# Kernel tuning notes

Hardware: AMD Instinct MI355X
Metric: run time of the kernel (lower is better)

The kernel has to match this reference:

```python
import jax, jax.numpy as jnp
import numpy as np

N, DEG, FIN, FOUT, K = 50000, 16, 32, 64, 3
E = N * DEG


def setup_inputs() -> dict:
    key = jax.random.key(0)
    ks = jax.random.split(key, 10)
    rng = np.random.default_rng(0)
    # unique edges sorted row-major (src*N+dst), ring guarantees deg_in/out>0
    ring = np.arange(N, dtype=np.int64) * N + (np.arange(N, dtype=np.int64) + 1) % N
    cand = np.unique(rng.integers(0, N * N, size=3 * E, dtype=np.int64))
    cand = np.setdiff1d(cand, ring, assume_unique=True)[: E - N]
    codes = np.sort(np.concatenate([cand, ring]))
    assert codes.shape[0] == E
    edge_index = jnp.asarray(np.stack([codes // N, codes % N]).astype(np.int32))
    X = jax.random.normal(ks[0], (N, FIN), jnp.float32)
    edge_weight = jax.random.uniform(ks[1], (E,), jnp.float32, 0.5, 1.5)
    cin = FIN + FOUT
    xav = float(np.sqrt(6.0 / (cin + FOUT)))
    def w(k):
        return jax.random.uniform(k, (2, K, cin, FOUT), jnp.float32, -xav, xav)
    return {
        'X': X, 'edge_index': edge_index, 'edge_weight': edge_weight,
        'Wz': w(ks[2]), 'bz': jnp.zeros((FOUT,), jnp.float32),
        'Wr': w(ks[3]), 'br': jnp.zeros((FOUT,), jnp.float32),
        'Wh': w(ks[4]), 'bh': jnp.zeros((FOUT,), jnp.float32),
    }


def _dconv(X, src, dst, rev_src, rev_dst, norm_out, norm_in, W, b):
    n = X.shape[0]
    def prop(x, s, d, nrm):  # out[d] += nrm * x[s]
        return jax.ops.segment_sum(nrm[:, None] * x[s], d, num_segments=n)
    H = X @ W[0, 0] + X @ W[1, 0]
    if W.shape[1] > 1:
        Tx1o = prop(X, src, dst, norm_out)
        Tx1i = prop(X, rev_src, rev_dst, norm_in)
        H = H + Tx1o @ W[0, 1] + Tx1i @ W[1, 1]
        for k in range(2, W.shape[1]):
            Tx1o = 2.0 * prop(Tx1o, src, dst, norm_out) - X
            Tx1i = 2.0 * prop(Tx1i, rev_src, rev_dst, norm_in) - X
            H = H + Tx1o @ W[0, k] + Tx1i @ W[1, k]
    return H + b


def reference(X, edge_index, edge_weight, Wz, bz, Wr, br, Wh, bh):
    n = X.shape[0]
    src, dst = edge_index[0], edge_index[1]
    deg_out = jax.ops.segment_sum(edge_weight, src, num_segments=n)
    deg_in = jax.ops.segment_sum(edge_weight, dst, num_segments=n)
    # faithful to original: both norms indexed by row (source)
    norm_out = 1.0 / deg_out[src]
    norm_in = 1.0 / deg_in[src]
    # reverse edges in dense_to_sparse(adj.T) order: sorted by (dst, src)
    order = jnp.argsort(dst.astype(jnp.int64) * n + src.astype(jnp.int64))
    rev_src, rev_dst = dst[order], src[order]
    H = jnp.zeros((n, Wz.shape[-1]), X.dtype)
    dc = lambda inp, W, b: _dconv(inp, src, dst, rev_src, rev_dst, norm_out, norm_in, W, b)
    Z = jax.nn.sigmoid(dc(jnp.concatenate([X, H], axis=1), Wz, bz))
    R = jax.nn.sigmoid(dc(jnp.concatenate([X, H], axis=1), Wr, br))
    H_tilde = jnp.tanh(dc(jnp.concatenate([X, H * R], axis=1), Wh, bh))
    return Z * H + (1.0 - Z) * H_tilde
```

## Files before the change

kernel.cpp:

```cpp
#include <hip/hip_runtime.h>
#include <hip/hip_fp16.h>
#include <cmath>

#define NN 50000
#define NE 800000
#define NBIN 391
#define NBLK 391
#define FCAP 3072
#define DST_HI 42949
#define SRC_CUT 33648

__device__ __forceinline__ unsigned short f2h(float f) {
  __half h = __float2half_rn(f);
  return *reinterpret_cast<unsigned short*>(&h);
}

typedef _Float16 half4 __attribute__((ext_vector_type(4)));
typedef float f32x4 __attribute__((ext_vector_type(4)));

__global__ __launch_bounds__(256) void k_aux(const float* __restrict__ X, const int* __restrict__ src,
                                             const int* __restrict__ dst, const float* __restrict__ ew,
                                             int* __restrict__ H,
                                             int* __restrict__ rptr, float* __restrict__ dout,
                                             const float* __restrict__ Wz, const float* __restrict__ Wh,
                                             unsigned short* __restrict__ WT, unsigned short* __restrict__ Xh,
                                             int* __restrict__ s0g) {
  __shared__ int hh[NBIN];
  __shared__ int s0l;
  int bid = blockIdx.x;
  int t = threadIdx.x;
  if (bid >= 667) {
    int h = bid - 667;
    hh[t] = 0;
    if (t + 256 < NBIN) hh[t + 256] = 0;
    if (t == 0) s0l = 0;
    __syncthreads();
    int my = 0;
#pragma unroll
    for (int r = 0; r < 8; ++r) {
      int e = h * 2048 + r * 256 + t;
      if (e < NE) {
        int d = dst[e];
        atomicAdd(&hh[d >> 7], 1);
        my += (d < DST_HI) ? 1 : 0;
        my += (d == DST_HI && src[e] < SRC_CUT) ? 1 : 0;
      }
    }
    atomicAdd(&s0l, my);
    __syncthreads();
    H[t * NBLK + h] = hh[t];
    if (t + 256 < NBIN) H[(t + 256) * NBLK + h] = hh[t + 256];
    if (t == 0) atomicAdd(s0g, s0l);
  } else if (bid < 196) {
    int i = bid * 256 + t;
    if (i >= NN) return;
    int lo = 0, hi = NE;
    while (lo < hi) { int m = (lo + hi) >> 1; if (src[m] < i) lo = m + 1; else hi = m; }
    int lo2 = lo, hi2 = NE;
    while (lo2 < hi2) { int m = (lo2 + hi2) >> 1; if (src[m] < i + 1) lo2 = m + 1; else hi2 = m; }
    rptr[i] = lo;
    if (i == NN - 1) rptr[NN] = lo2;
    float a = 0.f;
    for (int p = lo; p < lo2; ++p) a += ew[p];
    dout[i] = a;
  } else if (bid < 276) {
    int idx = (bid - 196) * 256 + t;
    int kk = idx >> 7, f = idx & 127;
    int blk = kk >> 5, c = kk & 31;
    const float* W = (f < 64) ? Wz : Wh;
    int fl = f & 63;
    float v;
    if (blk == 0)      v = W[c * 64 + fl] + W[18432 + c * 64 + fl];
    else if (blk == 1) v = W[6144 + c * 64 + fl];
    else if (blk == 2) v = W[18432 + 6144 + c * 64 + fl];
    else if (blk == 3) v = W[2 * 6144 + c * 64 + fl];
    else               v = W[18432 + 2 * 6144 + c * 64 + fl];
    WT[f * 160 + kk] = f2h(v);
  } else {
    int tt = (bid - 276) * 256 + t;
    int base = tt * 16;
    if (base >= NN * 32) return;
#pragma unroll
    for (int q = 0; q < 2; ++q) {
      const float4 a = *(const float4*)&X[base + q * 8];
      const float4 b = *(const float4*)&X[base + q * 8 + 4];
      ushort4 o1 = make_ushort4(f2h(a.x), f2h(a.y), f2h(a.z), f2h(a.w));
      ushort4 o2 = make_ushort4(f2h(b.x), f2h(b.y), f2h(b.z), f2h(b.w));
      *(ushort4*)&Xh[base + q * 8] = o1;
      *(ushort4*)&Xh[base + q * 8 + 4] = o2;
    }
  }
}

__global__ __launch_bounds__(512) void k_scanrow(int* __restrict__ H, int* __restrict__ rowtot) {
  __shared__ int tmp[512];
  int row = blockIdx.x;
  int t = threadIdx.x;
  int v = (t < NBLK) ? H[row * NBLK + t] : 0;
  tmp[t] = v;
  __syncthreads();
  for (int off = 1; off < 512; off <<= 1) {
    int u = (t >= (unsigned)off) ? tmp[t - off] : 0;
    __syncthreads();
    tmp[t] += u;
    __syncthreads();
  }
  if (t < NBLK) H[row * NBLK + t] = tmp[t] - v;
  if (t == 511) rowtot[row] = tmp[511];
}

__global__ __launch_bounds__(512) void k_part(const int* __restrict__ src, const int* __restrict__ dst,
                                              const int* __restrict__ P, const int* __restrict__ rowtot,
                                              unsigned long long* __restrict__ cmp64) {
  __shared__ int loc[NBIN];
  __shared__ int rs[512];
  __shared__ int rbase[NBIN];
  int h = blockIdx.x;
  int t = threadIdx.x;
  int v = (t < NBIN) ? rowtot[t] : 0;
  rs[t] = v;
  if (t < NBIN) loc[t] = 0;
  __syncthreads();
  for (int off = 1; off < 512; off <<= 1) {
    int u = (t >= (unsigned)off) ? rs[t - off] : 0;
    __syncthreads();
    rs[t] += u;
    __syncthreads();
  }
  if (t < NBIN) rbase[t] = rs[t] - v;
  __syncthreads();
#pragma unroll
  for (int r = 0; r < 4; ++r) {
    int e = h * 2048 + r * 512 + t;
    if (e < NE) {
      int d = dst[e];
      int bin = d >> 7;
      int rk = atomicAdd(&loc[bin], 1);
      int pos = rbase[bin] + P[bin * NBLK + h] + rk;
      cmp64[pos] = ((unsigned long long)(d & 127) << 48) |
                   ((unsigned long long)src[e] << 24) | (unsigned long long)e;
    }
  }
}

__global__ __launch_bounds__(512) void k_fine(const int* __restrict__ rowtot, const float* __restrict__ ew,
                                              const unsigned long long* __restrict__ cmp64,
                                              const int* __restrict__ rawsrc, const float* __restrict__ dout,
                                              const int* __restrict__ s0g,
                                              int* __restrict__ sp, float* __restrict__ din,
                                              int2* __restrict__ cnf, int2* __restrict__ cnr) {
  __shared__ unsigned long long a1[FCAP], a2[FCAP];
  __shared__ int fh[128], fcnt[128], fo[129];
  __shared__ int bs[2];
  int cb = blockIdx.x;
  int t = threadIdx.x;
  if (t < 64) {
    int s = 0;
    for (int i = t; i < cb; i += 64) s += rowtot[i];
    s += __shfl_xor(s, 32, 64); s += __shfl_xor(s, 16, 64); s += __shfl_xor(s, 8, 64);
    s += __shfl_xor(s, 4, 64);  s += __shfl_xor(s, 2, 64);  s += __shfl_xor(s, 1, 64);
    if (t == 0) { bs[0] = s; bs[1] = s + rowtot[cb]; }
  }
  if (t < 128) { fh[t] = 0; fcnt[t] = 0; }
  __syncthreads();
  int base = bs[0];
  int m = bs[1] - base;
  if (m > FCAP) m = FCAP;
  for (int i = t; i < m; i += 512) {
    unsigned long long it = cmp64[base + i];
    a1[i] = it;
    atomicAdd(&fh[(int)(it >> 48)], 1);
  }
  __syncthreads();
  if (t < 64) {
    int v0 = fh[t * 2], v1 = fh[t * 2 + 1];
    int pair = v0 + v1;
    int run = pair;
    for (int off = 1; off < 64; off <<= 1) {
      int v = __shfl_up(run, off, 64);
      if (t >= off) run += v;
    }
    int excl = run - pair;
    fo[t * 2] = excl; fo[t * 2 + 1] = excl + v0;
    if (t == 63) fo[128] = excl + pair;
  }
  __syncthreads();
  for (int i = t; i < m; i += 512) {
    unsigned long long it = a1[i];
    int b = (int)(it >> 48);
    int p2 = fo[b] + atomicAdd(&fcnt[b], 1);
    a2[p2] = it;
  }
  if (t < 128) {
    int d = cb * 128 + t;
    if (d <= NN) sp[d] = base + fo[t];
  }
  __syncthreads();
  const int s0 = s0g[0];
  for (int i = t; i < m; i += 512) {
    unsigned long long it = a2[i];
    int seg = (int)(it >> 48);
    int f0 = fo[seg], f1 = fo[seg + 1];
    int rank = 0;
    for (int q = f0; q < f1; ++q) rank += (a2[q] < it) ? 1 : 0;
    int e = (int)(it & 0xFFFFFF);
    int sc = (int)((it >> 24) & 0xFFFF);
    int d = cb * 128 + seg;
    cnf[base + i] = make_int2(sc, __float_as_int(1.0f / dout[sc]));
    int j = base + f0 + rank - s0; if (j < 0) j += NE;
    cnr[e] = make_int2(d, rawsrc[j]);
  }
  int nd = t >> 2, ln = t & 3;
  int d = cb * 128 + nd;
  if (d < NN) {
    float s = 0.f;
    int e0 = fo[nd], e1 = fo[nd + 1];
    for (int i = e0 + ln; i < e1; i += 4) s += ew[(int)(a2[i] & 0xFFFFFF)];
    s += __shfl_down(s, 2, 4);
    s += __shfl_down(s, 1, 4);
    if (ln == 0) din[d] = s;
  }
}

__global__ __launch_bounds__(256) void k_prop2(const unsigned short* __restrict__ inA, const int* __restrict__ rpA,
                                               const int2* __restrict__ cnA, const float* __restrict__ wiA,
                                               unsigned short* __restrict__ outAh,
                                               const unsigned short* __restrict__ inB, const int* __restrict__ rpB,
                                               const int2* __restrict__ cnB, const float* __restrict__ wiB,
                                               unsigned short* __restrict__ outBh,
                                               const float* __restrict__ sub, float mul) {
  int t = blockIdx.x * 256 + threadIdx.x;
  const int half = NN * 8;
  const unsigned short* in; const int* rp; const int2* cn; const float* wi; unsigned short* outh;
  if (t < half) { in = inA; rp = rpA; cn = cnA; wi = wiA; outh = outAh; }
  else          { in = inB; rp = rpB; cn = cnB; wi = wiB; outh = outBh; t -= half; }
  int r = t >> 3;
  if (r >= NN) return;
  int lane8 = t & 7;
  int c4 = lane8 * 4;
  int b = rp[r], e2 = rp[r + 1];
  float a0[4] = {0.f, 0.f, 0.f, 0.f}, a1[4] = {0.f, 0.f, 0.f, 0.f};
  int p = b;
#define GATH(cc, ww) { \
    uint2 bv = *(const uint2*)&in[(cc) * 32 + c4]; \
    float2 f01 = __half22float2(*(const __half2*)&bv.x); \
    float2 f23 = __half22float2(*(const __half2*)&bv.y); \
    float* a = (jj & 1) ? a1 : a0; \
    a[0] += (ww) * f01.x; a[1] += (ww) * f01.y; \
    a[2] += (ww) * f23.x; a[3] += (ww) * f23.y; }
  for (; p + 16 <= e2; p += 16) {
    int2 u = cn[p + lane8];
    int2 v = cn[p + 8 + lane8];
    float uw = wi ? (1.0f / wi[u.y]) : __int_as_float(u.y);
    float vw = wi ? (1.0f / wi[v.y]) : __int_as_float(v.y);
#pragma unroll
    for (int jj = 0; jj < 8; ++jj) {
      int col = __shfl(u.x, jj, 8);
      float w = __shfl(uw, jj, 8);
      GATH(col, w)
    }
#pragma unroll
    for (int jj = 0; jj < 8; ++jj) {
      int col = __shfl(v.x, jj, 8);
      float w = __shfl(vw, jj, 8);
      GATH(col, w)
    }
  }
  for (; p + 8 <= e2; p += 8) {
    int2 u = cn[p + lane8];
    float uw = wi ? (1.0f / wi[u.y]) : __int_as_float(u.y);
#pragma unroll
    for (int jj = 0; jj < 8; ++jj) {
      int col = __shfl(u.x, jj, 8);
      float w = __shfl(uw, jj, 8);
      GATH(col, w)
    }
  }
  for (int jj = 0; p < e2; ++p) {
    int2 c1 = cn[p];
    float w = wi ? (1.0f / wi[c1.y]) : __int_as_float(c1.y);
    GATH(c1.x, w)
  }
#undef GATH
  float ax = a0[0] + a1[0], ay = a0[1] + a1[1], az = a0[2] + a1[2], aw = a0[3] + a1[3];
  float4 o;
  if (sub) {
    const float4 s = *(const float4*)&sub[r * 32 + c4];
    o.x = mul * ax - s.x; o.y = mul * ay - s.y; o.z = mul * az - s.z; o.w = mul * aw - s.w;
  } else {
    o.x = ax; o.y = ay; o.z = az; o.w = aw;
  }
  ushort4 oh = make_ushort4(f2h(o.x), f2h(o.y), f2h(o.z), f2h(o.w));
  *(ushort4*)&outh[r * 32 + c4] = oh;
}

__global__ __launch_bounds__(256) void k_gemm(const unsigned short* __restrict__ Xh,
                                              const unsigned short* __restrict__ T1oh,
                                              const unsigned short* __restrict__ T1ih,
                                              const unsigned short* __restrict__ T2oh,
                                              const unsigned short* __restrict__ T2ih,
                                              const unsigned short* __restrict__ WT,
                                              const float* __restrict__ bz, const float* __restrict__ bh,
                                              float* __restrict__ out) {
  __shared__ unsigned short wlds[128 * 168];
  const int tid = threadIdx.x;
  for (int i = tid; i < 128 * 20; i += 256) {
    int n = i / 20, o = i % 20;
    *(uint4*)&wlds[n * 168 + o * 8] = *(const uint4*)&WT[n * 160 + o * 8];
  }
  __syncthreads();
  const int l = tid & 63, wid = tid >> 6;
  const int m0 = wid * 16;
  const int rb = blockIdx.x * 64;
  int grow = rb + m0 + (l & 15); if (grow >= NN) grow = NN - 1;
  const int kg = (l >> 4) * 4;
  f32x4 acc[8];
#pragma unroll
  for (int t = 0; t < 8; ++t) acc[t] = (f32x4){0.f, 0.f, 0.f, 0.f};
  const unsigned short* srcs[5] = {Xh, T1oh, T1ih, T2oh, T2ih};
#pragma unroll
  for (int s = 0; s < 5; ++s) {
    const unsigned short* A = srcs[s];
#pragma unroll
    for (int h2 = 0; h2 < 2; ++h2) {
      const int kk = h2 * 16;
      half4 af = *(const half4*)&A[grow * 32 + kk + kg];
      const int kglob = s * 32 + kk + kg;
#pragma unroll
      for (int t = 0; t < 8; ++t) {
        half4 bf = *(const half4*)&wlds[(t * 16 + (l & 15)) * 168 + kglob];
        acc[t] = __builtin_amdgcn_mfma_f32_16x16x16f16(af, bf, acc[t], 0, 0, 0);
      }
    }
  }
  const int c = l & 15;
#pragma unroll
  for (int t = 0; t < 4; ++t) {
    int col = t * 16 + c;
    float bzv = bz[col], bhv = bh[col];
#pragma unroll
    for (int i = 0; i < 4; ++i) {
      int r = rb + m0 + (l >> 4) * 4 + i;
      if (r < NN) {
        float z = 1.f / (1.f + expf(-(acc[t][i] + bzv)));
        float hv = tanhf(acc[t + 4][i] + bhv);
        out[r * 64 + col] = (1.f - z) * hv;
      }
    }
  }
}

extern "C" void kernel_launch(void* const* d_in, const int* in_sizes, int n_in,
                              void* d_out, int out_size, void* d_ws, size_t ws_size,
                              hipStream_t stream) {
  const float* X  = (const float*)d_in[0];
  const int*   ei = (const int*)d_in[1];
  const float* ew = (const float*)d_in[2];
  const float* Wz = (const float*)d_in[3];
  const float* bz = (const float*)d_in[4];
  const float* Wh = (const float*)d_in[7];
  const float* bh = (const float*)d_in[8];
  float* out = (float*)d_out;
  const int* src = ei;
  const int* dst = ei + NE;

  char* p = (char*)d_ws;
  auto alloc = [&](size_t bytes) -> char* {
    char* r = p;
    p += (bytes + 255) & ~(size_t)255;
    return r;
  };
  unsigned short* Xh   = (unsigned short*)alloc((size_t)NN * 32 * 2);
  unsigned short* T1oh = (unsigned short*)alloc((size_t)NN * 32 * 2);
  unsigned short* T1ih = (unsigned short*)alloc((size_t)NN * 32 * 2);
  unsigned short* T2oh = (unsigned short*)alloc((size_t)NN * 32 * 2);
  unsigned short* T2ih = (unsigned short*)alloc((size_t)NN * 32 * 2);
  unsigned long long* cmp64 = (unsigned long long*)alloc((size_t)NE * 8);
  int2*  cnf     = (int2*)alloc((size_t)NE * 8);
  int2*  cnr     = (int2*)alloc((size_t)NE * 8);
  int*   H       = (int*)alloc((size_t)NBIN * NBLK * 4);
  int*   rowtot  = (int*)alloc(NBIN * 4);
  int*   sp      = (int*)alloc((NN + 1) * 4);
  int*   rptr    = (int*)alloc((NN + 1) * 4);
  float* dout    = (float*)alloc(NN * 4);
  float* din     = (float*)alloc(NN * 4);
  unsigned short* WT = (unsigned short*)alloc(128 * 160 * 2);
  int*   s0g     = (int*)alloc(256);

  hipMemsetAsync(s0g, 0, 4, stream);
  k_aux<<<1058, 256, 0, stream>>>(X, src, dst, ew, H, rptr, dout, Wz, Wh, WT, Xh, s0g);
  k_scanrow<<<NBIN, 512, 0, stream>>>(H, rowtot);
  k_part<<<NBLK, 512, 0, stream>>>(src, dst, H, rowtot, cmp64);
  k_fine<<<NBIN, 512, 0, stream>>>(rowtot, ew, cmp64, src, dout, s0g, sp, din, cnf, cnr);

  k_prop2<<<3125, 256, 0, stream>>>(Xh, sp, cnf, nullptr, T1oh,
                                    Xh, rptr, cnr, din, T1ih, nullptr, 1.f);
  k_prop2<<<3125, 256, 0, stream>>>(T1oh, sp, cnf, nullptr, T2oh,
                                    T1ih, rptr, cnr, din, T2ih, X, 2.f);

  k_gemm<<<782, 256, 0, stream>>>(Xh, T1oh, T1ih, T2oh, T2ih, WT, bz, bh, out);
}
```

Baseline: 225.4 us.

## Replace histogram+scan partition with atomic bin reservation into fixed-capacity slots

Removes the global per-block histogram, the row-scan kernel and the prefix-sum inside the partition kernel. Each partition block now counts its local bins and reserves space with global atomics in fixed FCAP-sized slots per bin, and the s0 count moves into the same pass. This drops a kernel launch and the histogram traffic, but reads dst twice, uses a larger scratch buffer, and makes the order of edges within a bin nondeterministic. The fine kernel's prefix sum over earlier bins is kept to derive base offsets.

Result: no change. 224.5 us (-0.4%).

```diff
diff --git a/kernel.cpp b/kernel.cpp
--- a/kernel.cpp
+++ b/kernel.cpp
@@ -19,39 +19,13 @@
 typedef float f32x4 __attribute__((ext_vector_type(4)));
 
 __global__ __launch_bounds__(256) void k_aux(const float* __restrict__ X, const int* __restrict__ src,
-                                             const int* __restrict__ dst, const float* __restrict__ ew,
-                                             int* __restrict__ H,
+                                             const float* __restrict__ ew,
                                              int* __restrict__ rptr, float* __restrict__ dout,
                                              const float* __restrict__ Wz, const float* __restrict__ Wh,
-                                             unsigned short* __restrict__ WT, unsigned short* __restrict__ Xh,
-                                             int* __restrict__ s0g) {
-  __shared__ int hh[NBIN];
-  __shared__ int s0l;
+                                             unsigned short* __restrict__ WT, unsigned short* __restrict__ Xh) {
   int bid = blockIdx.x;
   int t = threadIdx.x;
-  if (bid >= 667) {
-    int h = bid - 667;
-    hh[t] = 0;
-    if (t + 256 < NBIN) hh[t + 256] = 0;
-    if (t == 0) s0l = 0;
-    __syncthreads();
-    int my = 0;
-#pragma unroll
-    for (int r = 0; r < 8; ++r) {
-      int e = h * 2048 + r * 256 + t;
-      if (e < NE) {
-        int d = dst[e];
-        atomicAdd(&hh[d >> 7], 1);
-        my += (d < DST_HI) ? 1 : 0;
-        my += (d == DST_HI && src[e] < SRC_CUT) ? 1 : 0;
-      }
-    }
-    atomicAdd(&s0l, my);
-    __syncthreads();
-    H[t * NBLK + h] = hh[t];
-    if (t + 256 < NBIN) H[(t + 256) * NBLK + h] = hh[t + 256];
-    if (t == 0) atomicAdd(s0g, s0l);
-  } else if (bid < 196) {
+  if (bid < 196) {
     int i = bid * 256 + t;
     if (i >= NN) return;
     int lo = 0, hi = NE;
@@ -92,58 +66,51 @@
   }
 }
 
-__global__ __launch_bounds__(512) void k_scanrow(int* __restrict__ H, int* __restrict__ rowtot) {
-  __shared__ int tmp[512];
-  int row = blockIdx.x;
-  int t = threadIdx.x;
-  int v = (t < NBLK) ? H[row * NBLK + t] : 0;
-  tmp[t] = v;
-  __syncthreads();
-  for (int off = 1; off < 512; off <<= 1) {
-    int u = (t >= (unsigned)off) ? tmp[t - off] : 0;
-    __syncthreads();
-    tmp[t] += u;
-    __syncthreads();
-  }
-  if (t < NBLK) H[row * NBLK + t] = tmp[t] - v;
-  if (t == 511) rowtot[row] = tmp[511];
-}
-
-__global__ __launch_bounds__(512) void k_part(const int* __restrict__ src, const int* __restrict__ dst,
-                                              const int* __restrict__ P, const int* __restrict__ rowtot,
-                                              unsigned long long* __restrict__ cmp64) {
+__global__ __launch_bounds__(512) void k_part2(const int* __restrict__ src, const int* __restrict__ dst,
+                                               int* __restrict__ gbin, int* __restrict__ s0g,
+                                               unsigned long long* __restrict__ cmp64) {
   __shared__ int loc[NBIN];
-  __shared__ int rs[512];
-  __shared__ int rbase[NBIN];
+  __shared__ int gbase[NBIN];
+  __shared__ int s0l;
   int h = blockIdx.x;
   int t = threadIdx.x;
-  int v = (t < NBIN) ? rowtot[t] : 0;
-  rs[t] = v;
   if (t < NBIN) loc[t] = 0;
-  __syncthreads();
-  for (int off = 1; off < 512; off <<= 1) {
-    int u = (t >= (unsigned)off) ? rs[t - off] : 0;
-    __syncthreads();
-    rs[t] += u;
-    __syncthreads();
-  }
-  if (t < NBIN) rbase[t] = rs[t] - v;
-  __syncthreads();
+  if (t == 0) s0l = 0;
+  __syncthreads();
+#pragma unroll
+  for (int r = 0; r < 4; ++r) {
+    int e = h * 2048 + r * 512 + t;
+    if (e < NE) atomicAdd(&loc[dst[e] >> 7], 1);
+  }
+  __syncthreads();
+  if (t < NBIN) {
+    int c = loc[t];
+    gbase[t] = (c > 0) ? atomicAdd(&gbin[t], c) : 0;
+    loc[t] = 0;
+  }
+  __syncthreads();
+  int my = 0;
 #pragma unroll
   for (int r = 0; r < 4; ++r) {
     int e = h * 2048 + r * 512 + t;
     if (e < NE) {
       int d = dst[e];
+      int s = src[e];
       int bin = d >> 7;
       int rk = atomicAdd(&loc[bin], 1);
-      int pos = rbase[bin] + P[bin * NBLK + h] + rk;
+      int pos = bin * FCAP + gbase[bin] + rk;
       cmp64[pos] = ((unsigned long long)(d & 127) << 48) |
-                   ((unsigned long long)src[e] << 24) | (unsigned long long)e;
-    }
-  }
-}
-
-__global__ __launch_bounds__(512) void k_fine(const int* __restrict__ rowtot, const float* __restrict__ ew,
+                   ((unsigned long long)s << 24) | (unsigned long long)e;
+      my += (d < DST_HI) ? 1 : 0;
+      my += (d == DST_HI && s < SRC_CUT) ? 1 : 0;
+    }
+  }
+  atomicAdd(&s0l, my);
+  __syncthreads();
+  if (t == 0) atomicAdd(s0g, s0l);
+}
+
+__global__ __launch_bounds__(512) void k_fine(const int* __restrict__ gbin, const float* __restrict__ ew,
                                               const unsigned long long* __restrict__ cmp64,
                                               const int* __restrict__ rawsrc, const float* __restrict__ dout,
                                               const int* __restrict__ s0g,
@@ -156,18 +123,19 @@
   int t = threadIdx.x;
   if (t < 64) {
     int s = 0;
-    for (int i = t; i < cb; i += 64) s += rowtot[i];
+    for (int i = t; i < cb; i += 64) s += gbin[i];
     s += __shfl_xor(s, 32, 64); s += __shfl_xor(s, 16, 64); s += __shfl_xor(s, 8, 64);
     s += __shfl_xor(s, 4, 64);  s += __shfl_xor(s, 2, 64);  s += __shfl_xor(s, 1, 64);
-    if (t == 0) { bs[0] = s; bs[1] = s + rowtot[cb]; }
+    if (t == 0) { bs[0] = s; bs[1] = gbin[cb]; }
   }
   if (t < 128) { fh[t] = 0; fcnt[t] = 0; }
   __syncthreads();
   int base = bs[0];
-  int m = bs[1] - base;
+  int m = bs[1];
   if (m > FCAP) m = FCAP;
+  const size_t slot = (size_t)cb * FCAP;
   for (int i = t; i < m; i += 512) {
-    unsigned long long it = cmp64[base + i];
+    unsigned long long it = cmp64[slot + i];
     a1[i] = it;
     atomicAdd(&fh[(int)(it >> 48)], 1);
   }
@@ -375,23 +343,21 @@
   unsigned short* T1ih = (unsigned short*)alloc((size_t)NN * 32 * 2);
   unsigned short* T2oh = (unsigned short*)alloc((size_t)NN * 32 * 2);
   unsigned short* T2ih = (unsigned short*)alloc((size_t)NN * 32 * 2);
-  unsigned long long* cmp64 = (unsigned long long*)alloc((size_t)NE * 8);
+  unsigned long long* cmp64 = (unsigned long long*)alloc((size_t)NBIN * FCAP * 8);
   int2*  cnf     = (int2*)alloc((size_t)NE * 8);
   int2*  cnr     = (int2*)alloc((size_t)NE * 8);
-  int*   H       = (int*)alloc((size_t)NBIN * NBLK * 4);
-  int*   rowtot  = (int*)alloc(NBIN * 4);
+  int*   gbin    = (int*)alloc((NBIN + 1) * 4);
   int*   sp      = (int*)alloc((NN + 1) * 4);
   int*   rptr    = (int*)alloc((NN + 1) * 4);
   float* dout    = (float*)alloc(NN * 4);
   float* din     = (float*)alloc(NN * 4);
   unsigned short* WT = (unsigned short*)alloc(128 * 160 * 2);
-  int*   s0g     = (int*)alloc(256);
-
-  hipMemsetAsync(s0g, 0, 4, stream);
-  k_aux<<<1058, 256, 0, stream>>>(X, src, dst, ew, H, rptr, dout, Wz, Wh, WT, Xh, s0g);
-  k_scanrow<<<NBIN, 512, 0, stream>>>(H, rowtot);
-  k_part<<<NBLK, 512, 0, stream>>>(src, dst, H, rowtot, cmp64);
-  k_fine<<<NBIN, 512, 0, stream>>>(rowtot, ew, cmp64, src, dout, s0g, sp, din, cnf, cnr);
+  int*   s0g     = gbin + NBIN;
+
+  hipMemsetAsync(gbin, 0, (NBIN + 1) * 4, stream);
+  k_aux<<<667, 256, 0, stream>>>(X, src, ew, rptr, dout, Wz, Wh, WT, Xh);
+  k_part2<<<NBLK, 512, 0, stream>>>(src, dst, gbin, s0g, cmp64);
+  k_fine<<<NBIN, 512, 0, stream>>>(gbin, ew, cmp64, src, dout, s0g, sp, din, cnf, cnr);
 
   k_prop2<<<3125, 256, 0, stream>>>(Xh, sp, cnf, nullptr, T1oh,
                                     Xh, rptr, cnr, din, T1ih, nullptr, 1.f);
```
